# Kernel optimization log

Hardware: AMD Instinct MI355X
Metric: run time of the kernel (lower is better)

The kernel has to match this reference:

```python
import jax, jax.numpy as jnp
import numpy as np

PATCH = 9          # patch_size
DILATION_PATCH = 1 # dilation_patch


def _bilinear_sample(img, px, py):
    """Bilinear sample img [b,c,H,W] at pixel coords px,py [b,P,h,w].
    Matches torch grid_sample(mode='bilinear', align_corners=True,
    padding_mode='zeros'): each out-of-bounds corner contributes zero.
    Returns [b,P,h,w,c]."""
    b, c, H, W = img.shape
    flat = img.transpose(0, 2, 3, 1).reshape(b, H * W, c)  # [b,HW,c]
    x0 = jnp.floor(px)
    y0 = jnp.floor(py)
    wx1 = px - x0
    wx0 = 1.0 - wx1
    wy1 = py - y0
    wy0 = 1.0 - wy1
    x0i = x0.astype(jnp.int32)
    y0i = y0.astype(jnp.int32)
    x1i = x0i + 1
    y1i = y0i + 1

    def gather(ix, iy):
        valid = ((ix >= 0) & (ix <= W - 1) & (iy >= 0) & (iy <= H - 1))
        idx = jnp.clip(iy, 0, H - 1) * W + jnp.clip(ix, 0, W - 1)  # [b,P,h,w]
        g = jnp.take_along_axis(flat, idx.reshape(b, -1, 1), axis=1)
        g = g.reshape(*ix.shape, c)
        return g * valid[..., None].astype(img.dtype)

    return ((wy0 * wx0)[..., None] * gather(x0i, y0i)
            + (wy0 * wx1)[..., None] * gather(x1i, y0i)
            + (wy1 * wx0)[..., None] * gather(x0i, y1i)
            + (wy1 * wx1)[..., None] * gather(x1i, y1i))


def setup_inputs() -> dict:
    key = jax.random.key(0)
    k1, k2, k3 = jax.random.split(key, 3)
    b, c, h, w = 2, 128, 64, 96
    return {
        "input1": jax.random.normal(k1, (b, c, h, w), dtype=jnp.float32),
        "input2": jax.random.normal(k2, (b, c, h, w), dtype=jnp.float32),
        "flow": jax.random.normal(k3, (b, 2, h, w), dtype=jnp.float32),
    }


def reference(input1, input2, flow):
    # kernel_size=1, stride=1, padding=0, dilation=1 (defaults supported by module)
    b, c, H, W = input2.shape
    dt = input1.dtype
    # absolute coordinate grid (x = horizontal, y = vertical), then translate by flow
    gy, gx = jnp.meshgrid(jnp.arange(H, dtype=dt), jnp.arange(W, dtype=dt), indexing='ij')
    cx = gx[None] + flow[:, 0]  # [b,h,w]
    cy = gy[None] + flow[:, 1]
    # patch offsets in pixels. The torch code normalizes to [-1,1] and samples with
    # align_corners=True, which is exactly equivalent to these pixel-space coords.
    off = DILATION_PATCH * ((PATCH - 1) // 2)
    offs = jnp.arange(PATCH, dtype=dt) * DILATION_PATCH - off
    dy, dx = jnp.meshgrid(offs, offs, indexing='ij')
    dy = dy.reshape(-1)  # [P]
    dx = dx.reshape(-1)
    px = cx[:, None] + dx[None, :, None, None]  # [b,P,h,w]
    py = cy[:, None] + dy[None, :, None, None]
    sampled = _bilinear_sample(input2, px, py)            # [b,P,h,w,c]
    corr = jnp.einsum('bphwc,bchw->bphw', sampled, input1)
    return corr.reshape(b, PATCH, PATCH, H, W)
```

## Files before the change

### kernel.cpp

```cpp
#include <hip/hip_runtime.h>

#define HH  64
#define WW  96
#define CC  128
#define BB  2
#define HWI (HH*WW)

#define PXB  8
#define TCOL 28
#define ROWB (TCOL*64)
#define BUFB (20*ROWB)
#define NCHK 35
#define AOFF BUFB
#define ASTR 272
#define LDSZ (AOFF + 16*ASTR)

typedef __attribute__((ext_vector_type(8))) _Float16 half8;
typedef __attribute__((ext_vector_type(4))) _Float16 half4;
typedef __attribute__((ext_vector_type(4))) float    f32x4;
typedef unsigned int u32;

__device__ __forceinline__ void gll16(const void* g, void* l) {
    __builtin_amdgcn_global_load_lds(
        (const __attribute__((address_space(1))) u32*)g,
        (__attribute__((address_space(3))) u32*)l, 16, 0, 0);
}

__global__ __launch_bounds__(256) void conv_i2(const float* __restrict__ I2,
                                               unsigned char* __restrict__ I2t)
{
    const int idx = blockIdx.x*256 + threadIdx.x;
    const int g   = idx & 3;
    const int L   = idx >> 2;
    const int col = L % WW;
    int t = L / WW;
    const int row = t & 63;  t >>= 6;
    const int kc  = t & 3;
    const int b   = t >> 2;
    const int slot = g ^ ((col ^ (col >> 2)) & 3);

    const float* src = I2 + ((size_t)(b*CC + kc*32 + g*8)*HH + row)*WW + col;
    half8 h;
#pragma unroll
    for (int j = 0; j < 8; ++j) h[j] = (_Float16)src[(size_t)j*HWI];
    *(half8*)(I2t + (size_t)L*64 + slot*16) = h;
}

__global__ __launch_bounds__(256, 4) void corr_kernel(
    const float* __restrict__ I1,
    const unsigned char* __restrict__ I2t,
    const float* __restrict__ flow,
    float* __restrict__ out)
{
    __shared__ __align__(16) unsigned char smem[LDSZ];

    const int tid  = threadIdx.x;
    const int lane = tid & 63;
    const int w    = tid >> 6;

    const int bid = blockIdx.x;
    const int xcd = bid & 7;
    const int j   = bid >> 3;
    const int b   = xcd >> 2;
    const int y0  = 16*(xcd & 3) + 2*(j & 7);
    const int X   = (j >> 3) * PXB;

    const int s_tile = min(max(X - 9, 0), WW - TCOL);

    const int fpx = lane & 15;
    const int kg  = lane >> 4;

    const int cpx = tid & 7;
    const int oq  = tid >> 3;
    const int xx  = X + cpx;
    float cxv[2], cyv[2];
#pragma unroll
    for (int yloc = 0; yloc < 2; ++yloc) {
        const int yy = y0 + yloc;
        cxv[yloc] = (float)xx + flow[((size_t)(b*2+0)*HH + yy)*WW + xx];
        cyv[yloc] = (float)yy + flow[((size_t)(b*2+1)*HH + yy)*WW + xx];
    }

#pragma unroll
    for (int i = 0; i < 2; ++i) {
        const int e   = tid + 256*i;
        const int q   = e & 1;
        const int ch  = (e >> 1) & 127;
        const int myy = e >> 8;
        const float4 v = *(const float4*)&I1[((size_t)(b*CC + ch)*HH + y0 + myy)*WW + X + q*4];
        const float ve[4] = { v.x, v.y, v.z, v.w };
#pragma unroll
        for (int k = 0; k < 4; ++k) {
            const int m = myy*8 + q*4 + k;
            *(_Float16*)(smem + AOFF + m*ASTR + ch*2) = (_Float16)ve[k];
        }
    }

    int boff[9];
#pragma unroll
    for (int i = 0; i < 9; ++i) {
        const int t   = min(w + 4*i, NCHK - 1);
        const int n   = t*16 + fpx;
        const int r_t = n / TCOL;
        const int c_t = n - r_t*TCOL;
        const int col = s_tile + c_t;
        boff[i] = r_t*ROWB + c_t*64 + ((kg ^ ((col ^ (col >> 2)) & 3)) << 4);
    }
    const int aoff = AOFF + fpx*ASTR + (kg << 4);

    auto stage = [&](int rr) {
#pragma unroll
        for (int i = 0; i < 9; ++i) {
            const int p = w + 4*i;
            if (p < NCHK) {
                const int z   = p*1024 + lane*16;
                const int r_t = z / ROWB;
                const int off = z - r_t*ROWB;
                const int c   = off >> 6;
                const int lb  = off & 63;
                const int grow = min(max(y0 - 9 + r_t, 0), HH - 1);
                const unsigned char* src = I2t
                    + ((size_t)(((b*4 + rr)*HH + grow)*WW + s_tile + c))*64 + lb;
                gll16(src, smem + p*1024);
            }
        }
    };

    f32x4 acc[9];
#pragma unroll
    for (int i = 0; i < 9; ++i) acc[i] = (f32x4){0.f,0.f,0.f,0.f};

    stage(0);
    __syncthreads();

#pragma unroll
    for (int r = 0; r < 4; ++r) {
        const half8 af = *(const half8*)(smem + aoff + r*64);
#pragma unroll
        for (int i = 0; i < 9; ++i) {
            if (w + 4*i < NCHK) {
                const half8 bf = *(const half8*)(smem + boff[i]);
                acc[i] = __builtin_amdgcn_mfma_f32_16x16x32_f16(af, bf, acc[i], 0, 0, 0);
            }
        }
        __syncthreads();
        if (r < 3) {
            stage(r + 1);
            __syncthreads();
        }
    }

    _Float16* D = (_Float16*)smem;
#pragma unroll
    for (int i = 0; i < 9; ++i) {
        if (w + 4*i < NCHK) {
            const int n   = (w + 4*i)*16 + fpx;
            const int r_t = n / TCOL;
            const int c_t = n - r_t*TCOL;
            const half4 hv = { (_Float16)acc[i][0], (_Float16)acc[i][1],
                               (_Float16)acc[i][2], (_Float16)acc[i][3] };
            *(half4*)(D + (c_t*21 + r_t)*20 + kg*4) = hv;
        }
    }
    __syncthreads();

#pragma unroll
    for (int yloc = 0; yloc < 2; ++yloc) {
        const int yy = y0 + yloc;
        const int m  = yloc*8 + cpx;
        const float cx = cxv[yloc], cy = cyv[yloc];
        const int x0c = (int)floorf(cx);
        const int y0c = (int)floorf(cy);
        const float wx1 = cx - (float)x0c, wx0 = 1.f - wx1;
        const float wy1 = cy - (float)y0c, wy0 = 1.f - wy1;
        float* outb = out + (size_t)b*81*HWI + (size_t)yy*WW + xx;

#pragma unroll
        for (int k = 0; k < 3; ++k) {
            const int o = oq + 32*k;
            if (o < 81) {
                const int dyi = o / 9;
                const int dxi = o - dyi*9;
                const int ix0 = x0c - 4 + dxi;
                const int iy0 = y0c - 4 + dyi;
                const bool vx0 = (ix0   >= 0) && (ix0   < WW);
                const bool vx1 = (ix0+1 >= 0) && (ix0+1 < WW);
                const bool vy0 = (iy0   >= 0) && (iy0   < HH);
                const bool vy1 = (iy0+1 >= 0) && (iy0+1 < HH);
                const int rt  = iy0 - y0 + 9;
                const int r0c = min(max(rt,     0), 19);
                const int r1c = min(max(rt + 1, 0), 19);
                const int c0  = ix0 - s_tile;
                const int c0c = min(max(c0,     0), TCOL-1);
                const int c1c = min(max(c0 + 1, 0), TCOL-1);
                const float d00 = (float)D[(c0c*21 + r0c)*20 + m];
                const float d01 = (float)D[(c1c*21 + r0c)*20 + m];
                const float d10 = (float)D[(c0c*21 + r1c)*20 + m];
                const float d11 = (float)D[(c1c*21 + r1c)*20 + m];
                const float r0 = (vx0 ? wx0*d00 : 0.f) + (vx1 ? wx1*d01 : 0.f);
                const float r1 = (vx0 ? wx0*d10 : 0.f) + (vx1 ? wx1*d11 : 0.f);
                const float v  = (vy0 ? wy0*r0 : 0.f) + (vy1 ? wy1*r1 : 0.f);
                outb[(size_t)o*HWI] = v;
            }
        }
    }
}

extern "C" void kernel_launch(void* const* d_in, const int* in_sizes, int n_in,
                              void* d_out, int out_size, void* d_ws, size_t ws_size,
                              hipStream_t stream)
{
    const float* I1   = (const float*)d_in[0];
    const float* I2   = (const float*)d_in[1];
    const float* flow = (const float*)d_in[2];
    float* out = (float*)d_out;
    unsigned char* I2t = (unsigned char*)d_ws;

    conv_i2<<<dim3(768), dim3(256), 0, stream>>>(I2, I2t);
    corr_kernel<<<dim3(768), dim3(256), 0, stream>>>(I1, I2t, flow, out);
}
```

Before: 20.04 us.

## Replicate converted input2 into per-XCD row-band slices with halo for L2 locality

The conversion kernel now writes the fp16 transposed input2 as eight per-XCD slices, each holding the 35-row band (with clamped halo) that the corr blocks scheduled on that XCD will read. The corr kernel indexes its XCD's slice directly, with no row clamping in the staging loop. The aim is to keep each XCD's reads within data it wrote, improving L2 locality and avoiding cross-XCD traffic. In exchange the conversion does more work and writes about 2.2x more data (1680 blocks instead of 768), and the layout relies on the block-to-XCD mapping being round-robin.

New measurement: 20.51 us. 2.4% more time.

```diff
diff --git a/kernel.cpp b/kernel.cpp
--- a/kernel.cpp
+++ b/kernel.cpp
@@ -14,6 +14,8 @@
 #define AOFF BUFB
 #define ASTR 272
 #define LDSZ (AOFF + 16*ASTR)
+#define SROWS 35
+#define SLICE (SROWS*WW)
 
 typedef __attribute__((ext_vector_type(8))) _Float16 half8;
 typedef __attribute__((ext_vector_type(4))) _Float16 half4;
@@ -29,21 +31,27 @@
 __global__ __launch_bounds__(256) void conv_i2(const float* __restrict__ I2,
                                                unsigned char* __restrict__ I2t)
 {
-    const int idx = blockIdx.x*256 + threadIdx.x;
-    const int g   = idx & 3;
-    const int L   = idx >> 2;
-    const int col = L % WW;
-    int t = L / WW;
-    const int row = t & 63;  t >>= 6;
-    const int kc  = t & 3;
-    const int b   = t >> 2;
+    const int bid = blockIdx.x;
+    const int tid = threadIdx.x;
+    const int xcd = bid & 7;
+    const int u   = (bid >> 3)*256 + tid;
+    const int g   = u & 3;
+    const int v   = u >> 2;
+    const int col = v % WW;
+    const int t2  = v / WW;
+    const int srow = t2 % SROWS;
+    const int kc   = t2 / SROWS;
+    const int b    = xcd >> 2;
+    const int band = xcd & 3;
+    const int grow = min(max(16*band - 9 + srow, 0), HH - 1);
+
+    const float* src = I2 + ((size_t)(b*CC + kc*32 + g*8)*HH + grow)*WW + col;
+    half8 h;
+#pragma unroll
+    for (int j = 0; j < 8; ++j) h[j] = (_Float16)src[(size_t)j*HWI];
+
     const int slot = g ^ ((col ^ (col >> 2)) & 3);
-
-    const float* src = I2 + ((size_t)(b*CC + kc*32 + g*8)*HH + row)*WW + col;
-    half8 h;
-#pragma unroll
-    for (int j = 0; j < 8; ++j) h[j] = (_Float16)src[(size_t)j*HWI];
-    *(half8*)(I2t + (size_t)L*64 + slot*16) = h;
+    *(half8*)(I2t + ((size_t)((xcd*4 + kc)*SLICE + srow*WW + col))*64 + slot*16) = h;
 }
 
 __global__ __launch_bounds__(256, 4) void corr_kernel(
@@ -66,6 +74,7 @@
     const int X   = (j >> 3) * PXB;
 
     const int s_tile = min(max(X - 9, 0), WW - TCOL);
+    const int srow0  = 2*(j & 7);
 
     const int fpx = lane & 15;
     const int kg  = lane >> 4;
@@ -108,6 +117,7 @@
     }
     const int aoff = AOFF + fpx*ASTR + (kg << 4);
 
+    const unsigned char* sbase = I2t + (size_t)(xcd*4)*SLICE*64;
     auto stage = [&](int rr) {
 #pragma unroll
         for (int i = 0; i < 9; ++i) {
@@ -118,9 +128,8 @@
                 const int off = z - r_t*ROWB;
                 const int c   = off >> 6;
                 const int lb  = off & 63;
-                const int grow = min(max(y0 - 9 + r_t, 0), HH - 1);
-                const unsigned char* src = I2t
-                    + ((size_t)(((b*4 + rr)*HH + grow)*WW + s_tile + c))*64 + lb;
+                const unsigned char* src = sbase
+                    + ((size_t)(rr*SLICE + (srow0 + r_t)*WW + s_tile + c))*64 + lb;
                 gll16(src, smem + p*1024);
             }
         }
@@ -216,6 +225,6 @@
     float* out = (float*)d_out;
     unsigned char* I2t = (unsigned char*)d_ws;
 
-    conv_i2<<<dim3(768), dim3(256), 0, stream>>>(I2, I2t);
+    conv_i2<<<dim3(1680), dim3(256), 0, stream>>>(I2, I2t);
     corr_kernel<<<dim3(768), dim3(256), 0, stream>>>(I1, I2t, flow, out);
 }
```
